# Kernel optimization log

Hardware: AMD Instinct MI355X
Metric: run time of the kernel (lower is better)

Reference implementation:

```python
import jax, jax.numpy as jnp
import numpy as np

N_EMBD = 1024
N_HEAD = 16
HEAD_DIM = N_EMBD // N_HEAD


def setup_inputs() -> dict:
    key = jax.random.key(0)
    ks = jax.random.split(key, 9)
    s = 1.0 / np.sqrt(N_EMBD)
    x = jax.random.normal(ks[0], (2, 2048, N_EMBD), dtype=jnp.float32)
    # PyTorch Linear weights stored as (out_features, in_features)
    Wq = jax.random.uniform(ks[1], (N_EMBD, N_EMBD), jnp.float32, -s, s)
    bq = jax.random.uniform(ks[2], (N_EMBD,), jnp.float32, -s, s)
    Wk = jax.random.uniform(ks[3], (N_EMBD, N_EMBD), jnp.float32, -s, s)
    bk = jax.random.uniform(ks[4], (N_EMBD,), jnp.float32, -s, s)
    Wv = jax.random.uniform(ks[5], (N_EMBD, N_EMBD), jnp.float32, -s, s)
    bv = jax.random.uniform(ks[6], (N_EMBD,), jnp.float32, -s, s)
    Wfc = jax.random.uniform(ks[7], (N_EMBD, N_EMBD), jnp.float32, -s, s)
    bfc = jax.random.uniform(ks[8], (N_EMBD,), jnp.float32, -s, s)
    return {"x": x, "Wq": Wq, "bq": bq, "Wk": Wk, "bk": bk,
            "Wv": Wv, "bv": bv, "Wfc": Wfc, "bfc": bfc}


def reference(x, Wq, bq, Wk, bk, Wv, bv, Wfc, bfc):
    B, S, _ = x.shape

    def proj(W, b):
        y = jnp.einsum('bsd,ed->bse', x, W) + b  # Linear: x @ W.T + b
        return y.reshape(B, S, N_HEAD, HEAD_DIM).transpose(0, 2, 1, 3)  # [B,H,S,Dh]

    q = proj(Wq, bq)
    k = proj(Wk, bk)
    v = proj(Wv, bv)
    scores = jnp.einsum('bhqd,bhkd->bhqk', q, k) / jnp.sqrt(jnp.float32(HEAD_DIM))
    weights = jax.nn.softmax(scores, axis=-1)  # [B,H,S,S]
    out = jnp.einsum('bhqk,bhkd->bhqd', weights, v)
    out = out.transpose(0, 2, 1, 3).reshape(B, S, N_EMBD)
    out = jnp.einsum('bsd,ed->bse', out, Wfc) + bfc
    return (out, weights)
```

## Files before the change

kernel.cpp:

```cpp
#include <hip/hip_runtime.h>
#include <hip/hip_bf16.h>
#include <stdint.h>


typedef __attribute__((ext_vector_type(8))) short bf16x8;
typedef __attribute__((ext_vector_type(4))) short bf16x4;
typedef __attribute__((ext_vector_type(4))) float f32x4;

#define MFMA16(a, b, c) __builtin_amdgcn_mfma_f32_16x16x32_bf16(a, b, c, 0, 0, 0)
#define EXP2(x) __builtin_amdgcn_exp2f(x)

__device__ __forceinline__ short f2bf(float x) {
  uint32_t u = __builtin_bit_cast(uint32_t, x);
  u += 0x7FFFu + ((u >> 16) & 1u);
  return (short)(u >> 16);
}

__device__ __forceinline__ uint32_t cvtpk_bf16(float lo, float hi) {
  uint32_t r;
  asm("v_cvt_pk_bf16_f32 %0, %1, %2" : "=v"(r) : "v"(lo), "v"(hi));
  return r;
}

__device__ __forceinline__ void gload16(const void* g, void* l) {
  __builtin_amdgcn_global_load_lds((const __attribute__((address_space(1))) uint32_t*)g,
                                   (__attribute__((address_space(3))) uint32_t*)l, 16, 0, 0);
}

__global__ __launch_bounds__(256) void cvt_k(const float* __restrict__ src,
                                             short* __restrict__ dst, int n4) {
  int i = blockIdx.x * 256 + threadIdx.x;
  if (i < n4) {
    f32x4 v = *(const f32x4*)(src + (size_t)i * 4);
    bf16x4 o;
    o[0] = f2bf(v[0]); o[1] = f2bf(v[1]); o[2] = f2bf(v[2]); o[3] = f2bf(v[3]);
    *(bf16x4*)(dst + (size_t)i * 4) = o;
  }
}

__global__ __launch_bounds__(256) void cvtw_k(
    const float* __restrict__ w0, const float* __restrict__ w1,
    const float* __restrict__ w2, const float* __restrict__ w3,
    short* __restrict__ dst) {
  const int which = blockIdx.x >> 10;
  const float* src = which == 0 ? w0 : which == 1 ? w1 : which == 2 ? w2 : w3;
  const int i = (blockIdx.x & 1023) * 256 + threadIdx.x;
  f32x4 v = *(const f32x4*)(src + (size_t)i * 4);
  bf16x4 o;
  o[0] = f2bf(v[0]); o[1] = f2bf(v[1]); o[2] = f2bf(v[2]); o[3] = f2bf(v[3]);
  *(bf16x4*)(dst + (size_t)which * 1048576 + (size_t)i * 4) = o;
}

template <int EPI>
__global__ __launch_bounds__(256) void gemm_k(
    const short* __restrict__ A, const short* __restrict__ B,
    const float* __restrict__ bq, const float* __restrict__ bk,
    const float* __restrict__ bv,
    short* __restrict__ Qb, short* __restrict__ Kb, short* __restrict__ Vt,
    float* __restrict__ Fout) {
  const int K = 1024;
  __shared__ short sA[128 * 32];
  __shared__ short sB[64 * 32];
  const int tid = threadIdx.x;
  const int w = tid >> 6, lane = tid & 63;
  const int wr = w >> 1, wc = w & 1;
  const int lrow = lane & 15, lk = (lane >> 4) * 8;
  const int tileM = blockIdx.x * 128, tileN = blockIdx.y * 64;

  f32x4 acc[4][2];
#pragma unroll
  for (int i = 0; i < 4; ++i)
#pragma unroll
    for (int j = 0; j < 2; ++j) acc[i][j] = (f32x4){0.f, 0.f, 0.f, 0.f};

  for (int k0 = 0; k0 < K; k0 += 32) {
#pragma unroll
    for (int i = 0; i < 2; ++i) {
      int u = (w * 2 + i) * 64 + lane;
      int row = u >> 2, c8 = (u & 3) * 8;
      gload16(A + (size_t)(tileM + row) * K + k0 + c8, (short*)sA + (w * 2 + i) * 512);
    }
    {
      int u = w * 64 + lane;
      int row = u >> 2, c8 = (u & 3) * 8;
      gload16(B + (size_t)(tileN + row) * K + k0 + c8, (short*)sB + w * 512);
    }
    __syncthreads();
    bf16x8 af[4], bfr[2];
#pragma unroll
    for (int mi = 0; mi < 4; ++mi)
      af[mi] = *(const bf16x8*)&sA[(wr * 64 + mi * 16 + lrow) * 32 + lk];
#pragma unroll
    for (int ni = 0; ni < 2; ++ni)
      bfr[ni] = *(const bf16x8*)&sB[(wc * 32 + ni * 16 + lrow) * 32 + lk];
#pragma unroll
    for (int mi = 0; mi < 4; ++mi)
#pragma unroll
      for (int ni = 0; ni < 2; ++ni)
        acc[mi][ni] = MFMA16(af[mi], bfr[ni], acc[mi][ni]);
    __syncthreads();
  }

#pragma unroll
  for (int mi = 0; mi < 4; ++mi) {
    int m0 = tileM + wr * 64 + mi * 16 + (lane >> 4) * 4;
#pragma unroll
    for (int ni = 0; ni < 2; ++ni) {
      int n = tileN + wc * 32 + ni * 16 + lrow;
      f32x4 v = acc[mi][ni];
      if (EPI == 0) {
        int which = n >> 10, e = n & 1023;
        int h = e >> 6, dh = e & 63;
        float bias = (which == 0 ? bq : which == 1 ? bk : bv)[e];
        int b = m0 >> 11, s0 = m0 & 2047;
        size_t hb = (size_t)(b * 16 + h);
        if (which == 2) {
          int kt2 = s0 >> 5, gl = (s0 >> 3) & 3, ni2 = dh >> 4, j = dh & 15;
          size_t base = (((hb * 64 + kt2) * 4 + ni2) * 64 + gl * 16 + j) * 8 + (s0 & 7);
          bf16x4 pk;
#pragma unroll
          for (int r = 0; r < 4; ++r) pk[r] = f2bf(v[r] + bias);
          *(bf16x4*)&Vt[base] = pk;
        } else {
          short* dst = (which == 0) ? Qb : Kb;
          int tile = s0 >> 4, h2 = dh >> 5, gl = (dh >> 3) & 3, ci = dh & 7;
          size_t base = (((hb * 128 + tile) * 2 + h2) * 64 + gl * 16 + (s0 & 15)) * 8 + ci;
#pragma unroll
          for (int r = 0; r < 4; ++r) dst[base + r * 8] = f2bf(v[r] + bias);
        }
      } else {
        float bias = bq[n];
#pragma unroll
        for (int r = 0; r < 4; ++r)
          Fout[(size_t)(m0 + r) * 1024 + n] = v[r] + bias;
      }
    }
  }
}

__device__ __forceinline__ void sw1_phase(bf16x8& pa, bf16x8& pb, int nxt,
    const short* __restrict__ Kf, int l8, const bf16x8& aQ0, const bf16x8& aQ1,
    float kscale, float& ls0, float& ls1, float& ls2, float& ls3) {
  const f32x4 zero = {0.f, 0.f, 0.f, 0.f};
  f32x4 s = MFMA16(pa, aQ0, zero);
  s = MFMA16(pb, aQ1, s);
  pa = *(const bf16x8*)&Kf[nxt * 1024 + l8];
  pb = *(const bf16x8*)&Kf[nxt * 1024 + 512 + l8];
  ls0 += EXP2(s[0] * kscale);
  ls1 += EXP2(s[1] * kscale);
  ls2 += EXP2(s[2] * kscale);
  ls3 += EXP2(s[3] * kscale);
}

__device__ __forceinline__ void sw2_phase(
    bf16x8& k00, bf16x8& k01, bf16x8& k10, bf16x8& k11,
    bf16x8& v0, bf16x8& v1, bf16x8& v2, bf16x8& v3,
    int kt2, int nxt, short* __restrict__ wl,
    const short* __restrict__ Kw, const short* __restrict__ Vw, int l8,
    const bf16x8& aQ0, const bf16x8& aQ1, float rl, float kscale,
    float* __restrict__ Wqp, int lrow, int g,
    f32x4& o0, f32x4& o1, f32x4& o2, f32x4& o3) {
  const f32x4 zero = {0.f, 0.f, 0.f, 0.f};
  f32x4 sa = MFMA16(k00, aQ0, zero);
  sa = MFMA16(k01, aQ1, sa);
  f32x4 sb = MFMA16(k10, aQ0, zero);
  sb = MFMA16(k11, aQ1, sb);
  const short* Ktn = &Kw[nxt * 2048];
  k00 = *(const bf16x8*)&Ktn[l8];
  k01 = *(const bf16x8*)&Ktn[512 + l8];
  k10 = *(const bf16x8*)&Ktn[1024 + l8];
  k11 = *(const bf16x8*)&Ktn[1536 + l8];
  f32x4 ea, eb;
#pragma unroll
  for (int r = 0; r < 4; ++r) ea[r] = EXP2(sa[r] * kscale) * rl;
#pragma unroll
  for (int r = 0; r < 4; ++r) eb[r] = EXP2(sb[r] * kscale) * rl;
  uint2 pa, pb;
  pa.x = cvtpk_bf16(ea[0], ea[1]);
  pa.y = cvtpk_bf16(ea[2], ea[3]);
  pb.x = cvtpk_bf16(eb[0], eb[1]);
  pb.y = cvtpk_bf16(eb[2], eb[3]);
  *(uint2*)&wl[lrow * 40 + g * 4] = pa;
  *(uint2*)&wl[lrow * 40 + 16 + g * 4] = pb;
  const bf16x8 aW = *(const bf16x8*)&wl[lrow * 40 + g * 8];
  o0 = MFMA16(aW, v0, o0);
  o1 = MFMA16(aW, v1, o1);
  o2 = MFMA16(aW, v2, o2);
  o3 = MFMA16(aW, v3, o3);
  const short* Vpn = &Vw[nxt * 2048];
  v0 = *(const bf16x8*)&Vpn[l8];
  v1 = *(const bf16x8*)&Vpn[512 + l8];
  v2 = *(const bf16x8*)&Vpn[1024 + l8];
  v3 = *(const bf16x8*)&Vpn[1536 + l8];
  *(f32x4*)&Wqp[kt2 * 32] = ea;
  *(f32x4*)&Wqp[kt2 * 32 + 16] = eb;
}

__global__ __launch_bounds__(256, 4) void attn_k(
    const short* __restrict__ Qb, const short* __restrict__ Kb,
    const short* __restrict__ Vt, float* __restrict__ Wout,
    short* __restrict__ attn) {
  __shared__ short Wlds[4][2][16 * 40];
  const int i = blockIdx.x;
  const int bh = ((i & 7) << 2) | ((i >> 3) & 3);
  const int qt = i >> 5;
  const int w = threadIdx.x >> 6, lane = threadIdx.x & 63;
  const int lrow = lane & 15, g = lane >> 4;
  const int qb = qt * 4 + w;
  const int l8 = lane * 8;
  const short* Qf = Qb + (size_t)(bh * 128 + qb) * 1024;
  const short* Kf = Kb + (size_t)bh * (128 * 1024);
  const short* Vf = Vt + (size_t)bh * (64 * 2048);
  const float kscale = 0.125f * 1.44269504088896f;
  const f32x4 zero = {0.f, 0.f, 0.f, 0.f};

  const bf16x8 aQ0 = *(const bf16x8*)&Qf[l8];
  const bf16x8 aQ1 = *(const bf16x8*)&Qf[512 + l8];

  float ls0 = 0.f, ls1 = 0.f, ls2 = 0.f, ls3 = 0.f;
  bf16x8 p0a = *(const bf16x8*)&Kf[0 * 1024 + l8];
  bf16x8 p0b = *(const bf16x8*)&Kf[0 * 1024 + 512 + l8];
  bf16x8 p1a = *(const bf16x8*)&Kf[1 * 1024 + l8];
  bf16x8 p1b = *(const bf16x8*)&Kf[1 * 1024 + 512 + l8];
  bf16x8 p2a = *(const bf16x8*)&Kf[2 * 1024 + l8];
  bf16x8 p2b = *(const bf16x8*)&Kf[2 * 1024 + 512 + l8];
  bf16x8 p3a = *(const bf16x8*)&Kf[3 * 1024 + l8];
  bf16x8 p3b = *(const bf16x8*)&Kf[3 * 1024 + 512 + l8];
  for (int kt = 0; kt < 128; kt += 4) {
    sw1_phase(p0a, p0b, (kt + 4) & 127, Kf, l8, aQ0, aQ1, kscale, ls0, ls1, ls2, ls3);
    sw1_phase(p1a, p1b, (kt + 5) & 127, Kf, l8, aQ0, aQ1, kscale, ls0, ls1, ls2, ls3);
    sw1_phase(p2a, p2b, (kt + 6) & 127, Kf, l8, aQ0, aQ1, kscale, ls0, ls1, ls2, ls3);
    sw1_phase(p3a, p3b, (kt + 7) & 127, Kf, l8, aQ0, aQ1, kscale, ls0, ls1, ls2, ls3);
  }
  float lsum = (ls0 + ls1) + (ls2 + ls3);
  lsum += __shfl_xor(lsum, 16);
  lsum += __shfl_xor(lsum, 32);
  const float rl = 1.0f / lsum;

  f32x4 o0 = zero, o1 = zero, o2 = zero, o3 = zero;
  float* Wqp = Wout + ((size_t)bh * 2048 + qb * 16 + lrow) * 2048 + g * 4;
  short* wlA = &Wlds[w][0][0];
  short* wlB = &Wlds[w][1][0];
  bf16x8 ka00 = *(const bf16x8*)&Kf[l8],        ka01 = *(const bf16x8*)&Kf[512 + l8];
  bf16x8 ka10 = *(const bf16x8*)&Kf[1024 + l8], ka11 = *(const bf16x8*)&Kf[1536 + l8];
  bf16x8 va0 = *(const bf16x8*)&Vf[l8],         va1 = *(const bf16x8*)&Vf[512 + l8];
  bf16x8 va2 = *(const bf16x8*)&Vf[1024 + l8],  va3 = *(const bf16x8*)&Vf[1536 + l8];
  bf16x8 kb00 = *(const bf16x8*)&Kf[2048 + l8], kb01 = *(const bf16x8*)&Kf[2560 + l8];
  bf16x8 kb10 = *(const bf16x8*)&Kf[3072 + l8], kb11 = *(const bf16x8*)&Kf[3584 + l8];
  bf16x8 vb0 = *(const bf16x8*)&Vf[2048 + l8],  vb1 = *(const bf16x8*)&Vf[2560 + l8];
  bf16x8 vb2 = *(const bf16x8*)&Vf[3072 + l8],  vb3 = *(const bf16x8*)&Vf[3584 + l8];
  for (int kt2 = 0; kt2 < 64; kt2 += 2) {
    sw2_phase(ka00, ka01, ka10, ka11, va0, va1, va2, va3,
              kt2, (kt2 + 2) & 63, wlA, Kf, Vf, l8, aQ0, aQ1, rl, kscale,
              Wqp, lrow, g, o0, o1, o2, o3);
    sw2_phase(kb00, kb01, kb10, kb11, vb0, vb1, vb2, vb3,
              kt2 + 1, (kt2 + 3) & 63, wlB, Kf, Vf, l8, aQ0, aQ1, rl, kscale,
              Wqp, lrow, g, o0, o1, o2, o3);
  }

  const int b = bh >> 4, h = bh & 15;
  const size_t obase = (size_t)(b * 2048 + qb * 16 + g * 4) * 1024 + h * 64 + lrow;
#pragma unroll
  for (int r = 0; r < 4; ++r) {
    attn[obase + (size_t)r * 1024 +  0] = f2bf(o0[r]);
    attn[obase + (size_t)r * 1024 + 16] = f2bf(o1[r]);
    attn[obase + (size_t)r * 1024 + 32] = f2bf(o2[r]);
    attn[obase + (size_t)r * 1024 + 48] = f2bf(o3[r]);
  }
}

extern "C" void kernel_launch(void* const* d_in, const int* in_sizes, int n_in,
                              void* d_out, int out_size, void* d_ws,
                              size_t ws_size, hipStream_t stream) {
  const float* x   = (const float*)d_in[0];
  const float* Wq  = (const float*)d_in[1];
  const float* bq  = (const float*)d_in[2];
  const float* Wk  = (const float*)d_in[3];
  const float* bk  = (const float*)d_in[4];
  const float* Wv  = (const float*)d_in[5];
  const float* bv  = (const float*)d_in[6];
  const float* Wfc = (const float*)d_in[7];
  const float* bfc = (const float*)d_in[8];

  float* out  = (float*)d_out;
  float* wout = out + (size_t)4194304;

  char* ws = (char*)d_ws;
  short* xb   = (short*)(ws);
  short* wqkv = (short*)(ws + ((size_t)8  << 20));
  short* wfcb = (short*)(ws + ((size_t)14 << 20));
  short* Qb   = (short*)(ws + ((size_t)16 << 20));
  short* Kb   = (short*)(ws + ((size_t)24 << 20));
  short* Vt   = (short*)(ws + ((size_t)32 << 20));
  short* attn = xb;

  cvt_k<<<4096, 256, 0, stream>>>(x, xb, 1048576);
  cvtw_k<<<4096, 256, 0, stream>>>(Wq, Wk, Wv, Wfc, wqkv);

  gemm_k<0><<<dim3(32, 48), 256, 0, stream>>>(xb, wqkv, bq, bk, bv, Qb, Kb, Vt,
                                              (float*)nullptr);

  attn_k<<<dim3(1024), 256, 0, stream>>>(Qb, Kb, Vt, wout, attn);

  gemm_k<1><<<dim3(32, 16), 256, 0, stream>>>(attn, wfcb, bfc, nullptr, nullptr,
                                              nullptr, nullptr, nullptr, out);
}
```

Baseline: 266.5 us.

## Software-pipeline PV MFMA one step behind QK and merge conversion kernels

The attention second pass now issues the P·V MFMAs for the previous tile before computing the current tile's exp and LDS write. This spaces out the LDS write/read dependency and overlaps the exp work with the matrix ops. A prologue and an epilogue are added for the first and last tiles. Separately, the x and weight fp32-to-bf16 conversion kernels are merged into one launch to save a kernel launch.

```diff
diff --git a/kernel.cpp b/kernel.cpp
--- a/kernel.cpp
+++ b/kernel.cpp
@@ -27,28 +27,28 @@
                                    (__attribute__((address_space(3))) uint32_t*)l, 16, 0, 0);
 }
 
-__global__ __launch_bounds__(256) void cvt_k(const float* __restrict__ src,
-                                             short* __restrict__ dst, int n4) {
-  int i = blockIdx.x * 256 + threadIdx.x;
-  if (i < n4) {
-    f32x4 v = *(const f32x4*)(src + (size_t)i * 4);
-    bf16x4 o;
-    o[0] = f2bf(v[0]); o[1] = f2bf(v[1]); o[2] = f2bf(v[2]); o[3] = f2bf(v[3]);
-    *(bf16x4*)(dst + (size_t)i * 4) = o;
-  }
-}
-
-__global__ __launch_bounds__(256) void cvtw_k(
+__global__ __launch_bounds__(256) void cvtall_k(
+    const float* __restrict__ x,
     const float* __restrict__ w0, const float* __restrict__ w1,
     const float* __restrict__ w2, const float* __restrict__ w3,
-    short* __restrict__ dst) {
-  const int which = blockIdx.x >> 10;
-  const float* src = which == 0 ? w0 : which == 1 ? w1 : which == 2 ? w2 : w3;
-  const int i = (blockIdx.x & 1023) * 256 + threadIdx.x;
-  f32x4 v = *(const f32x4*)(src + (size_t)i * 4);
+    short* __restrict__ xb, short* __restrict__ wb) {
+  const size_t i = (size_t)blockIdx.x * 256 + threadIdx.x;
+  const float* src;
+  short* dst;
+  if (i < 1048576) {
+    src = x + i * 4;
+    dst = xb + i * 4;
+  } else {
+    const size_t j = i - 1048576;
+    const int which = (int)(j >> 18);
+    const float* w = which == 0 ? w0 : which == 1 ? w1 : which == 2 ? w2 : w3;
+    src = w + (j & 262143) * 4;
+    dst = wb + j * 4;
+  }
+  f32x4 v = *(const f32x4*)src;
   bf16x4 o;
   o[0] = f2bf(v[0]); o[1] = f2bf(v[1]); o[2] = f2bf(v[2]); o[3] = f2bf(v[3]);
-  *(bf16x4*)(dst + (size_t)which * 1048576 + (size_t)i * 4) = o;
+  *(bf16x4*)dst = o;
 }
 
 template <int EPI>
@@ -152,7 +152,8 @@
   ls3 += EXP2(s[3] * kscale);
 }
 
-__device__ __forceinline__ void sw2_phase(
+template <bool DOPV>
+__device__ __forceinline__ void sw2p(
     bf16x8& k00, bf16x8& k01, bf16x8& k10, bf16x8& k11,
     bf16x8& v0, bf16x8& v1, bf16x8& v2, bf16x8& v3,
     int kt2, int nxt, short* __restrict__ wl,
@@ -165,6 +166,13 @@
   sa = MFMA16(k01, aQ1, sa);
   f32x4 sb = MFMA16(k10, aQ0, zero);
   sb = MFMA16(k11, aQ1, sb);
+  if (DOPV) {
+    const bf16x8 aW = *(const bf16x8*)&wl[lrow * 40 + g * 8];
+    o0 = MFMA16(aW, v0, o0);
+    o1 = MFMA16(aW, v1, o1);
+    o2 = MFMA16(aW, v2, o2);
+    o3 = MFMA16(aW, v3, o3);
+  }
   const short* Ktn = &Kw[nxt * 2048];
   k00 = *(const bf16x8*)&Ktn[l8];
   k01 = *(const bf16x8*)&Ktn[512 + l8];
@@ -182,12 +190,7 @@
   pb.y = cvtpk_bf16(eb[2], eb[3]);
   *(uint2*)&wl[lrow * 40 + g * 4] = pa;
   *(uint2*)&wl[lrow * 40 + 16 + g * 4] = pb;
-  const bf16x8 aW = *(const bf16x8*)&wl[lrow * 40 + g * 8];
-  o0 = MFMA16(aW, v0, o0);
-  o1 = MFMA16(aW, v1, o1);
-  o2 = MFMA16(aW, v2, o2);
-  o3 = MFMA16(aW, v3, o3);
-  const short* Vpn = &Vw[nxt * 2048];
+  const short* Vpn = &Vw[kt2 * 2048];
   v0 = *(const bf16x8*)&Vpn[l8];
   v1 = *(const bf16x8*)&Vpn[512 + l8];
   v2 = *(const bf16x8*)&Vpn[1024 + l8];
@@ -243,19 +246,36 @@
   short* wlB = &Wlds[w][1][0];
   bf16x8 ka00 = *(const bf16x8*)&Kf[l8],        ka01 = *(const bf16x8*)&Kf[512 + l8];
   bf16x8 ka10 = *(const bf16x8*)&Kf[1024 + l8], ka11 = *(const bf16x8*)&Kf[1536 + l8];
-  bf16x8 va0 = *(const bf16x8*)&Vf[l8],         va1 = *(const bf16x8*)&Vf[512 + l8];
-  bf16x8 va2 = *(const bf16x8*)&Vf[1024 + l8],  va3 = *(const bf16x8*)&Vf[1536 + l8];
   bf16x8 kb00 = *(const bf16x8*)&Kf[2048 + l8], kb01 = *(const bf16x8*)&Kf[2560 + l8];
   bf16x8 kb10 = *(const bf16x8*)&Kf[3072 + l8], kb11 = *(const bf16x8*)&Kf[3584 + l8];
-  bf16x8 vb0 = *(const bf16x8*)&Vf[2048 + l8],  vb1 = *(const bf16x8*)&Vf[2560 + l8];
-  bf16x8 vb2 = *(const bf16x8*)&Vf[3072 + l8],  vb3 = *(const bf16x8*)&Vf[3584 + l8];
-  for (int kt2 = 0; kt2 < 64; kt2 += 2) {
-    sw2_phase(ka00, ka01, ka10, ka11, va0, va1, va2, va3,
-              kt2, (kt2 + 2) & 63, wlA, Kf, Vf, l8, aQ0, aQ1, rl, kscale,
-              Wqp, lrow, g, o0, o1, o2, o3);
-    sw2_phase(kb00, kb01, kb10, kb11, vb0, vb1, vb2, vb3,
-              kt2 + 1, (kt2 + 3) & 63, wlB, Kf, Vf, l8, aQ0, aQ1, rl, kscale,
-              Wqp, lrow, g, o0, o1, o2, o3);
+  bf16x8 va0, va1, va2, va3, vb0, vb1, vb2, vb3;
+  sw2p<false>(ka00, ka01, ka10, ka11, va0, va1, va2, va3,
+              0, 2, wlA, Kf, Vf, l8, aQ0, aQ1, rl, kscale, Wqp, lrow, g,
+              o0, o1, o2, o3);
+  sw2p<false>(kb00, kb01, kb10, kb11, vb0, vb1, vb2, vb3,
+              1, 3, wlB, Kf, Vf, l8, aQ0, aQ1, rl, kscale, Wqp, lrow, g,
+              o0, o1, o2, o3);
+  for (int kt2 = 2; kt2 < 64; kt2 += 2) {
+    sw2p<true>(ka00, ka01, ka10, ka11, va0, va1, va2, va3,
+               kt2, (kt2 + 2) & 63, wlA, Kf, Vf, l8, aQ0, aQ1, rl, kscale,
+               Wqp, lrow, g, o0, o1, o2, o3);
+    sw2p<true>(kb00, kb01, kb10, kb11, vb0, vb1, vb2, vb3,
+               kt2 + 1, (kt2 + 3) & 63, wlB, Kf, Vf, l8, aQ0, aQ1, rl, kscale,
+               Wqp, lrow, g, o0, o1, o2, o3);
+  }
+  {
+    const bf16x8 aW = *(const bf16x8*)&wlA[lrow * 40 + g * 8];
+    o0 = MFMA16(aW, va0, o0);
+    o1 = MFMA16(aW, va1, o1);
+    o2 = MFMA16(aW, va2, o2);
+    o3 = MFMA16(aW, va3, o3);
+  }
+  {
+    const bf16x8 aW = *(const bf16x8*)&wlB[lrow * 40 + g * 8];
+    o0 = MFMA16(aW, vb0, o0);
+    o1 = MFMA16(aW, vb1, o1);
+    o2 = MFMA16(aW, vb2, o2);
+    o3 = MFMA16(aW, vb3, o3);
   }
 
   const int b = bh >> 4, h = bh & 15;
@@ -294,8 +314,7 @@
   short* Vt   = (short*)(ws + ((size_t)32 << 20));
   short* attn = xb;
 
-  cvt_k<<<4096, 256, 0, stream>>>(x, xb, 1048576);
-  cvtw_k<<<4096, 256, 0, stream>>>(Wq, Wk, Wv, Wfc, wqkv);
+  cvtall_k<<<8192, 256, 0, stream>>>(x, Wq, Wk, Wv, Wfc, xb, wqkv);
 
   gemm_k<0><<<dim3(32, 48), 256, 0, stream>>>(xb, wqkv, bq, bk, bv, Qb, Kb, Vt,
                                               (float*)nullptr);
```

New measurement: 263.2 us. About the same (-1.2%).
